# Optimization experiments

Measured on AMD Instinct MI355X. Metric: run time of the kernel, lower is better.

Reference implementation:

```python
import jax, jax.numpy as jnp
import numpy as np
from collections import deque

SIGMA_LOW = 0.02  # TreeFilter2D(sigma=0.02); high-level trees use sigma=1 (low_tree=False)


def bilinear_resize(x, oh, ow):
    # torch F.interpolate(mode='bilinear', align_corners=False)
    B, C, H, W = x.shape
    sy, sx = H / oh, W / ow
    ys = jnp.maximum((jnp.arange(oh, dtype=jnp.float32) + 0.5) * sy - 0.5, 0.0)
    xs = jnp.maximum((jnp.arange(ow, dtype=jnp.float32) + 0.5) * sx - 0.5, 0.0)
    y0 = jnp.clip(jnp.floor(ys).astype(jnp.int32), 0, H - 1)
    x0 = jnp.clip(jnp.floor(xs).astype(jnp.int32), 0, W - 1)
    y1 = jnp.minimum(y0 + 1, H - 1)
    x1 = jnp.minimum(x0 + 1, W - 1)
    wy = (ys - y0).reshape(oh, 1)
    wx = (xs - x0).reshape(1, ow)
    top, bot = x[:, :, y0, :], x[:, :, y1, :]
    v00, v01 = top[:, :, :, x0], top[:, :, :, x1]
    v10, v11 = bot[:, :, :, x0], bot[:, :, :, x1]
    return ((1 - wy) * (1 - wx)) * v00 + ((1 - wy) * wx) * v01 + (wy * (1 - wx)) * v10 + (wy * wx) * v11


def nearest_resize(x, oh, ow):
    B, C, H, W = x.shape
    yi = jnp.minimum((jnp.arange(oh) * (H / oh)).astype(jnp.int32), H - 1)
    xi = jnp.minimum((jnp.arange(ow) * (W / ow)).astype(jnp.int32), W - 1)
    return x[:, :, yi, :][:, :, :, xi]


def _mst_adj(feat, h, w):
    # Kruskal MST on 4-connected grid; edge weight = norm2_distance of features.
    n = h * w
    idx = np.arange(n).reshape(h, w)
    eu = np.concatenate([idx[:, :-1].ravel(), idx[:-1, :].ravel()])
    ev = np.concatenate([idx[:, 1:].ravel(), idx[1:, :].ravel()])
    f = feat.reshape(feat.shape[0], -1).astype(np.float64)
    d = ((f[:, eu] - f[:, ev]) ** 2).sum(axis=0)
    order = np.argsort(d, kind='stable')
    pa = np.arange(n)

    def find(a):
        r = a
        while pa[r] != r:
            r = pa[r]
        while pa[a] != r:
            pa[a], a = r, pa[a]
        return r

    adj = [[] for _ in range(n)]
    cnt = 0
    for e in order:
        u, v = int(eu[e]), int(ev[e])
        ru, rv = find(u), find(v)
        if ru != rv:
            pa[ru] = rv
            adj[u].append(v)
            adj[v].append(u)
            cnt += 1
            if cnt == n - 1:
                break
    return adj


def build_forest(embed):
    # embed: np [B,C,h,w] -> global parent array (ids b*n+i) + per-BFS-level node lists
    B, C, h, w = embed.shape
    n = h * w
    parent = np.arange(B * n)
    level = np.zeros(B * n, dtype=np.int64)
    for b in range(B):
        adj = _mst_adj(embed[b], h, w)
        lv = np.full(n, -1, dtype=np.int64)
        lv[0] = 0
        q = deque([0])
        while q:
            u = q.popleft()
            for v in adj[u]:
                if lv[v] < 0:
                    lv[v] = lv[u] + 1
                    parent[b * n + v] = b * n + u
                    q.append(v)
        level[b * n:(b + 1) * n] = lv
    d = int(level.max())
    levels = [np.nonzero(level == l)[0] for l in range(1, d + 1)]
    return jnp.asarray(parent), levels


def tree_filter(feature, embed, parent, levels, sigma):
    # feature [B,C,n], embed [B,Ce,n]; normalized tree filtering:
    # y_i = sum_j prod(path-edge-weights) x_j / sum_j prod(path-edge-weights)
    B, C, n = feature.shape
    ones = jnp.ones((B, 1, n), feature.dtype)
    xg = jnp.moveaxis(jnp.concatenate([feature, ones], axis=1), 0, 1).reshape(C + 1, B * n)
    eg = jnp.moveaxis(embed, 0, 1).reshape(embed.shape[1], B * n)
    wgt = jnp.exp(-((eg - eg[:, parent]) ** 2).sum(axis=0) / sigma)  # [B*n]; root entries unused
    # upward (leaf->root) subtree aggregation
    A = xg
    for idx in reversed(levels):
        A = A.at[:, parent[idx]].add(wgt[idx] * A[:, idx])
    # downward (root->leaf) completion
    F = A
    for idx in levels:
        F = F.at[:, idx].set(A[:, idx] + wgt[idx] * (F[:, parent[idx]] - wgt[idx] * A[:, idx]))
    y = F[:C] / F[C]
    return jnp.moveaxis(y.reshape(C, B, n), 0, 1)  # [B,C,n]


def setup_inputs() -> dict:
    key = jax.random.key(0)
    ks = jax.random.split(key, 6)
    B, K, h, w = 8, 4, 48, 48
    C = 512
    preds = jax.random.normal(ks[0], (B, K, h, w), jnp.float32)
    low_feats = jax.random.uniform(ks[1], (B, 3, 192, 192), jnp.float32) * 0.1
    hf1 = jax.random.normal(ks[2], (B, C, 24, 24), jnp.float32) * 0.05
    hf2 = jax.random.normal(ks[3], (B, C, 12, 12), jnp.float32) * 0.05
    hf3 = jax.random.normal(ks[4], (B, C, 6, 6), jnp.float32) * 0.05
    rois = (jax.random.uniform(ks[5], (B, 192, 192)) > 0.5).astype(jnp.float32)
    weight = jnp.asarray(0.4, jnp.float32)
    return {"preds": preds, "low_feats": low_feats, "high_feats_1": hf1,
            "high_feats_2": hf2, "high_feats_3": hf3, "unlabeled_ROIs": rois,
            "weight": weight}


def reference(preds, low_feats, high_feats_1, high_feats_2, high_feats_3, unlabeled_ROIs, weight):
    B, K, h, w = preds.shape
    low = bilinear_resize(low_feats, h, w)                     # no_grad in original
    roi = nearest_resize(unlabeled_ROIs[:, None], h, w)        # [B,1,h,w]
    N = roi.sum()
    prob = jax.nn.softmax(preds, axis=1)
    probf = prob.reshape(B, K, -1)
    roif = roi.reshape(B, 1, -1)

    parent0, lv0 = build_forest(np.asarray(low))
    AS = tree_filter(probf, low.reshape(B, low.shape[1], -1), parent0, lv0, SIGMA_LOW)

    loss = jnp.zeros((), preds.dtype)
    for hf in (high_feats_1, high_feats_2, high_feats_3):
        hfi = bilinear_resize(hf, h, w)
        p, lv = build_forest(np.asarray(hfi))
        AS_k = tree_filter(AS, hfi.reshape(B, hfi.shape[1], -1), p, lv, 1.0)
        loss = loss + (roif * jnp.abs(probf - AS_k)).sum()
    loss = jnp.where(N > 0, loss / N, loss)
    return weight * loss
```

## Files before the change

### kernel.cpp

```cpp
#include <hip/hip_runtime.h>
#include <math.h>


#define HH 48
#define WW 48
#define NN (HH*WW)
#define EHH (HH*(WW-1))
#define EEE (2*EHH)
#define BB 8
#define KK 4
#define TPB 256
#define TPE 512
#define TPW 1024
#define TPR 1024
#define TPF 512
#define NPL 5
#define NHE ((EHH+TPE-1)/TPE)
#define ESLOT (4*NN)
#define LVE (2*(NN-1))
#define RIPT ((LVE+TPR-1)/TPR)
#define SENTN 0xFFFFu
#define MAXT 12

#define SSTRIDE_W (4*NN+8)
#define PK_OFF 0
#define D_OFF (4*NN)

__device__ __forceinline__ void edge_uv(int e,int& u,int& v){
  if(e<EHH){ int r=e/(WW-1); int c=e-r*(WW-1); u=r*WW+c; v=u+1; }
  else     { int t=e-EHH; u=t; v=t+WW; }
}

__device__ __forceinline__ void pick_src(int f, const float* lowf, const float* hf1,
                                         const float* hf2, const float* hf3,
                                         const float*& src, int& sh, int& C){
  if(f==0){src=lowf; sh=192; C=3;}
  else if(f==1){src=hf1; sh=24; C=512;}
  else if(f==2){src=hf2; sh=12; C=512;}
  else        {src=hf3; sh=6;  C=512;}
}

__global__ __launch_bounds__(TPB) void k_prob(const float* __restrict__ preds,
                                              float* __restrict__ probf){
  int t=blockIdx.x*TPB+threadIdx.x;
  if(t>=BB*NN) return;
  int b=t/NN, i=t-b*NN;
  const float* p=preds+(size_t)b*KK*NN+i;
  float x0=p[0],x1=p[NN],x2=p[2*NN],x3=p[3*NN];
  float mx=fmaxf(fmaxf(x0,x1),fmaxf(x2,x3));
  float e0=expf(x0-mx),e1=expf(x1-mx),e2=expf(x2-mx),e3=expf(x3-mx);
  float s=((e0+e1)+(e2+e3));
  float* q=probf+(size_t)b*KK*NN+i;
  q[0]=e0/s; q[NN]=e1/s; q[2*NN]=e2/s; q[3*NN]=e3/s;
}

__global__ __launch_bounds__(TPE) void k_edges(
  const float* __restrict__ lowf, const float* __restrict__ hf1,
  const float* __restrict__ hf2, const float* __restrict__ hf3,
  double* __restrict__ pd_low, double* __restrict__ pd_hf, int nchunk)
{
  __shared__ float up[4*NN];
  __shared__ int   y0t[48], y1t[48];
  __shared__ float wyt[48];
  const int tid=threadIdx.x;
  int pidx, chunk, hfidx=0;
  if(blockIdx.x<8){ pidx=blockIdx.x; chunk=0; }
  else { int t=blockIdx.x-8; hfidx=t/nchunk; chunk=t-hfidx*nchunk; pidx=8+hfidx; }
  const int f=pidx>>3, b=pidx&7;
  const float* src; int sh,C;
  pick_src(f,lowf,hf1,hf2,hf3,src,sh,C);
  const int shw=sh*sh;
  const float* srcb=src+(size_t)b*C*shw;
  const int cpc=(f==0)?3:(512/nchunk);
  const int c_begin=chunk*cpc;
  const int c_end=(c_begin+cpc<C)?(c_begin+cpc):C;

  if(tid<48){
    float sy=(float)sh/48.0f;
    float ys=fmaxf(((float)tid+0.5f)*sy-0.5f,0.0f);
    int y0=(int)ys; if(y0>sh-1) y0=sh-1;
    int y1=y0+1; if(y1>sh-1) y1=sh-1;
    y0t[tid]=y0; y1t[tid]=y1; wyt[tid]=ys-(float)y0;
  }

  double accH[NHE], accV[NHE];
  #pragma unroll
  for(int j=0;j<NHE;j++){ accH[j]=0.0; accV[j]=0.0; }

  for(int c0=c_begin;c0<c_end;c0+=4){
    const int nc=(c_end-c0<4)?(c_end-c0):4;
    __syncthreads();
    for(int i=tid;i<NN;i+=TPE){
      int r=i/WW, c=i-r*WW;
      int y0=y0t[r], y1=y1t[r]; float wy=wyt[r];
      int x0=y0t[c], x1=y1t[c]; float wx=wyt[c];
      float w00=(1.0f-wy)*(1.0f-wx), w01=(1.0f-wy)*wx;
      float w10=wy*(1.0f-wx),        w11=wy*wx;
      int o00=y0*sh+x0, o01=y0*sh+x1, o10=y1*sh+x0, o11=y1*sh+x1;
      const float* pl=srcb+(size_t)c0*shw;
      for(int cc=0;cc<nc;cc++){
        const float* p=pl+(size_t)cc*shw;
        up[cc*NN+i]=w00*p[o00]+w01*p[o01]+w10*p[o10]+w11*p[o11];
      }
    }
    __syncthreads();
    for(int j=0;j<NHE;j++){
      int e=tid+j*TPE;
      if(e<EHH){
        int r=e/(WW-1); int u=r*WW+(e-r*(WW-1));
        const float* pu=up+u;
        for(int c=0;c<nc;c++){
          double d=(double)pu[c*NN]-(double)pu[c*NN+1];
          accH[j]=fma(d,d,accH[j]);
        }
      }
    }
    for(int j=0;j<NHE;j++){
      int u=tid+j*TPE;
      if(u<EHH){
        const float* pu=up+u;
        for(int c=0;c<nc;c++){
          double d=(double)pu[c*NN]-(double)pu[c*NN+WW];
          accV[j]=fma(d,d,accV[j]);
        }
      }
    }
  }
  double* outp=(f==0)? pd_low+(size_t)pidx*EEE
                     : pd_hf+((size_t)hfidx*nchunk+chunk)*EEE;
  #pragma unroll
  for(int j=0;j<NHE;j++){
    int e=tid+j*TPE;
    if(e<EHH){ outp[e]=accH[j]; outp[EHH+e]=accV[j]; }
  }
}

__global__ __launch_bounds__(TPB) void k_redux(
  const double* __restrict__ pd_low, const double* __restrict__ pd_hf,
  int nchunk, double* __restrict__ dkeyG)
{
  int t=blockIdx.x*TPB+threadIdx.x;
  if(t>=32*EEE) return;
  int pidx=t/EEE, e=t-pidx*EEE;
  double s;
  if(pidx<8) s=pd_low[(size_t)pidx*EEE+e];
  else {
    const double* p0=pd_hf+((size_t)(pidx-8)*nchunk)*EEE+e;
    s=0.0;
    for(int k=0;k<nchunk;k++) s+=p0[(size_t)k*EEE];
  }
  dkeyG[t]=s;
}

__global__ __launch_bounds__(TPW) void k_boruvka(
  const double* __restrict__ dkeyG,
  float4* __restrict__ adjwG, unsigned char* __restrict__ adjG)
{
  __shared__ double dkey[EEE];
  __shared__ unsigned long long bestd[NN];
  __shared__ int comp[NN];
  __shared__ int lnk[NN];
  __shared__ int beste[NN];
  __shared__ unsigned char mstf[EEE];
  __shared__ int flags[2];

  const int tid=threadIdx.x;
  const int pidx=blockIdx.x;
  const int f=pidx>>3;
  const float sigma=(f==0)?0.02f:1.0f;

  const double* p0=dkeyG+(size_t)pidx*EEE;
  for(int e=tid;e<EEE;e+=TPW) dkey[e]=p0[e];
  for(int i=tid;i<NN;i+=TPW) comp[i]=i;
  for(int e=tid;e<EEE;e+=TPW) mstf[e]=0;
  __syncthreads();

  for(int round=0;round<20;++round){
    for(int i=tid;i<NN;i+=TPW){ bestd[i]=~0ull; beste[i]=0x7fffffff; lnk[i]=i; }
    if(tid==0) flags[1]=0;
    __syncthreads();
    for(int e=tid;e<EEE;e+=TPW){
      int u,v; edge_uv(e,u,v);
      int cu=comp[u], cv=comp[v];
      if(cu!=cv){
        unsigned long long db=(unsigned long long)__double_as_longlong(dkey[e]);
        atomicMin(&bestd[cu],db);
        atomicMin(&bestd[cv],db);
      }
    }
    __syncthreads();
    for(int e=tid;e<EEE;e+=TPW){
      int u,v; edge_uv(e,u,v);
      int cu=comp[u], cv=comp[v];
      if(cu!=cv){
        unsigned long long db=(unsigned long long)__double_as_longlong(dkey[e]);
        if(db==bestd[cu]) atomicMin(&beste[cu],e);
        if(db==bestd[cv]) atomicMin(&beste[cv],e);
      }
    }
    __syncthreads();
    for(int i=tid;i<NN;i+=TPW){
      if(comp[i]==i && beste[i]!=0x7fffffff){
        int e=beste[i]; int u,v; edge_uv(e,u,v);
        int cu=comp[u], cv=comp[v];
        int other=(cu==i)?cv:cu;
        bool mutual=(beste[other]==e);
        if(!mutual || other<i){ lnk[i]=other; mstf[e]=1; flags[1]=1; }
      }
    }
    __syncthreads();
    if(flags[1]==0) break;
    {
      volatile int* vl=lnk;
      for(int i=tid;i<NN;i+=TPW){
        int x=comp[i];
        int p=vl[x];
        int gp=vl[p];
        while(p!=gp){
          vl[x]=gp;
          x=p; p=gp; gp=vl[p];
        }
        comp[i]=p;
      }
    }
    __syncthreads();
  }

  for(int i=tid;i<NN;i+=TPW){
    int r=i/WW, c=i-r*WW;
    int mask=0; float4 w; w.x=0.0f; w.y=0.0f; w.z=0.0f; w.w=0.0f;
    if(c>0    && mstf[r*(WW-1)+c-1]){ mask|=1; w.x=expf(-(float)dkey[r*(WW-1)+c-1]/sigma); }
    if(c<WW-1 && mstf[r*(WW-1)+c])  { mask|=2; w.y=expf(-(float)dkey[r*(WW-1)+c]/sigma); }
    if(r>0    && mstf[EHH+i-WW])    { mask|=4; w.z=expf(-(float)dkey[EHH+i-WW]/sigma); }
    if(r<HH-1 && mstf[EHH+i])       { mask|=8; w.w=expf(-(float)dkey[EHH+i]/sigma); }
    adjwG[(size_t)pidx*NN+i]=w;
    adjG[(size_t)pidx*NN+i]=(unsigned char)mask;
  }
}

__global__ __launch_bounds__(TPR) void k_root(
  const float4* __restrict__ adjwG, const unsigned char* __restrict__ adjG,
  int* __restrict__ sbase)
{
  __shared__ unsigned int eA[ESLOT];
  __shared__ unsigned int eB[ESLOT];
  __shared__ float4 adjwS[NN];
  __shared__ unsigned char adjS[NN];
  __shared__ int chunkS[TPR];
  __shared__ int maxdS;

  const int tid=threadIdx.x;
  const int pidx=blockIdx.x;
  {
    const float4* aw=adjwG+(size_t)pidx*NN;
    for(int t=tid;t<NN;t+=TPR) adjwS[t]=aw[t];
    const int* a4=(const int*)(adjG+(size_t)pidx*NN);
    int* s4=(int*)adjS;
    for(int t=tid;t<NN/4;t+=TPR) s4[t]=a4[t];
  }
  if(tid==0) maxdS=0;
  __syncthreads();

  const int m0=adjS[0];
  const int d0=(m0&1)?0:((m0&2)?1:((m0&4)?2:3));
  const int e0=d0;

  for(int t=tid;t<ESLOT;t+=TPR){
    int u=t>>2, d=t&3;
    unsigned int pk=0;
    if(adjS[u]&(1<<d)){
      int v=(d==0)?u-1:(d==1)?u+1:(d==2)?u-WW:u+WW;
      int rd=d^1;
      int mv=adjS[v];
      int nd=rd;
      #pragma unroll
      for(int k2=4;k2>=1;k2--){ int dd=(rd+k2)&3; if(mv&(1<<dd)) nd=dd; }
      int ne=(v<<2)|nd;
      unsigned int nxt=(ne==e0)?SENTN:(unsigned int)ne;
      pk=(nxt<<16)|1u;
    }
    eA[t]=pk;
  }
  __syncthreads();

  unsigned int* P=eA; unsigned int* Q=eB;
  for(int r2=0;r2<13;r2++){
    for(int t=tid;t<ESLOT;t+=TPR){
      unsigned int pk=P[t];
      unsigned int dist=pk&0xFFFFu, nxt=pk>>16;
      if(dist && nxt!=SENTN){
        unsigned int pk2=P[nxt];
        dist+=pk2&0xFFFFu;
        nxt=pk2>>16;
        pk=(nxt<<16)|dist;
      }
      Q[t]=pk;
    }
    __syncthreads();
    unsigned int* tmp=P; P=Q; Q=tmp;
  }
  for(int t=tid;t<ESLOT;t+=TPR){
    unsigned int dist=P[t]&0xFFFFu;
    Q[t]=dist?(unsigned int)(LVE-(int)dist):0xFFFFFFFFu;
  }
  __syncthreads();

  int* scanA=(int*)P;
  for(int t=tid;t<ESLOT;t+=TPR){
    unsigned int pos=Q[t];
    if(pos!=0xFFFFFFFFu){
      int u=t>>2, d=t&3;
      int v=(d==0)?u-1:(d==1)?u+1:(d==2)?u-WW:u+WW;
      unsigned int rpos=Q[(v<<2)|(d^1)];
      scanA[pos]=(pos<rpos)?1:-1;
    }
  }
  __syncthreads();

  const int base=tid*RIPT;
  int vals[RIPT]; int lsum=0;
  #pragma unroll
  for(int j=0;j<RIPT;j++){
    int p=base+j;
    int v=(p<LVE)?scanA[p]:0;
    lsum+=v; vals[j]=lsum;
  }
  chunkS[tid]=lsum;
  __syncthreads();
  for(int off=1;off<TPR;off<<=1){
    int v=chunkS[tid];
    int vv=(tid>=off)?chunkS[tid-off]:0;
    __syncthreads();
    chunkS[tid]=v+vv;
    __syncthreads();
  }
  const int myoff=(tid>0)?chunkS[tid-1]:0;
  int mymax=0;
  #pragma unroll
  for(int j=0;j<RIPT;j++){
    int p=base+j;
    if(p<LVE){ int s=vals[j]+myoff; scanA[p]=s; if(s>mymax) mymax=s; }
  }
  if(mymax>0) atomicMax(&maxdS,mymax);
  __syncthreads();

  int* sp=sbase+(size_t)pidx*SSTRIDE_W;
  int4* g_pk=(int4*)(sp+PK_OFF);
  if(tid==0){
    g_pk[0]=make_int4(0,__float_as_int(0.0f),0,0);
    sp[D_OFF]=maxdS;
  }
  for(int t=tid;t<ESLOT;t+=TPR){
    unsigned int pos=Q[t];
    if(pos!=0xFFFFFFFFu){
      int u=t>>2, d=t&3;
      int v=(d==0)?u-1:(d==1)?u+1:(d==2)?u-WW:u+WW;
      unsigned int rpos=Q[(v<<2)|(d^1)];
      if(pos<rpos){
        float4 w4=adjwS[u];
        float w=(d==0)?w4.x:(d==1)?w4.y:(d==2)?w4.z:w4.w;
        g_pk[v]=make_int4(u,__float_as_int(w),scanA[pos],0);
      }
    }
  }
}

__global__ __launch_bounds__(TPF) void k_tables(
  const int* __restrict__ sbase, int* __restrict__ ancT,
  float* __restrict__ prodT)
{
  __shared__ int   ancA[NN], ancB[NN];
  __shared__ float prmA[NN], prmB[NN];
  const int tid=threadIdx.x;
  const int pidx=blockIdx.x;
  const int* sp=sbase+(size_t)pidx*SSTRIDE_W;
  const int4* g_pk=(const int4*)(sp+PK_OFF);
  const int maxD=sp[D_OFF];
  int T=1; while((1<<T)<=maxD) T++;
  int* gA=ancT+(size_t)pidx*MAXT*NN;
  float* gP=prodT+(size_t)pidx*MAXT*NN;
  int* aP=ancA; int* aQ=ancB; float* pP=prmA; float* pQ=prmB;
  for(int i=tid;i<NN;i+=TPF){
    int4 rec=g_pk[i];
    aP[i]=rec.x; pP[i]=__int_as_float(rec.y);
    gA[i]=rec.x; gP[i]=pP[i];
  }
  __syncthreads();
  for(int t=1;t<T;t++){
    for(int i=tid;i<NN;i+=TPF){
      int a=aP[i];
      int a2=aP[a]; float pr=pP[i]*pP[a];
      aQ[i]=a2; pQ[i]=pr;
      gA[(size_t)t*NN+i]=a2; gP[(size_t)t*NN+i]=pr;
    }
    __syncthreads();
    { int* t1=aP; aP=aQ; aQ=t1; float* t2=pP; pP=pQ; pQ=t2; }
  }
}

__global__ __launch_bounds__(TPF) void k_fchan(
  const float* __restrict__ X, float* __restrict__ Fout,
  const int* __restrict__ sbase, const int* __restrict__ ancT,
  const float* __restrict__ prodT, int pidx0)
{
  __shared__ float S[NN];
  __shared__ float Sb[NN];
  const int tid=threadIdx.x;
  const int pg=blockIdx.x/5, c=blockIdx.x%5;
  const int pidx=pidx0+pg;
  const int xb=pg&7;
  const int* sp=sbase+(size_t)pidx*SSTRIDE_W;
  const int4* g_pk=(const int4*)(sp+PK_OFF);
  const int maxD=sp[D_OFF];
  int T=1; while((1<<T)<=maxD) T++;
  const int* ancP=ancT+(size_t)pidx*MAXT*NN;
  const float* prmP=prodT+(size_t)pidx*MAXT*NN;

  int dep[NPL]; float wv[NPL];
  #pragma unroll
  for(int j=0;j<NPL;j++){
    int i=tid+j*TPF;
    if(i<NN){
      int4 rec=g_pk[i];
      dep[j]=rec.z; wv[j]=__int_as_float(rec.y);
      S[i]=(c<4)? X[((size_t)xb*KK+c)*NN+i] : 1.0f;
    } else { dep[j]=-1; wv[j]=0.0f; }
  }
  __syncthreads();

  for(int t=0;t<T;t++){
    float sn[NPL]; int aj[NPL]; float pj[NPL];
    #pragma unroll
    for(int j=0;j<NPL;j++){
      int i=tid+j*TPF;
      if(i<NN){ sn[j]=S[i]; aj[j]=ancP[(size_t)t*NN+i]; pj[j]=prmP[(size_t)t*NN+i]; }
      else { sn[j]=0.0f; aj[j]=0; pj[j]=0.0f; }
    }
    __syncthreads();
    int bit=1<<t;
    #pragma unroll
    for(int j=0;j<NPL;j++){
      if(dep[j]>=bit) atomicAdd(&S[aj[j]], pj[j]*sn[j]);
    }
    __syncthreads();
  }

  #pragma unroll
  for(int j=0;j<NPL;j++){
    int i=tid+j*TPF;
    if(i<NN){ float fq=1.0f-wv[j]*wv[j]; Sb[i]=fq*S[i]; }
  }
  __syncthreads();

  float* Sp=Sb; float* Sq=S;
  for(int t=0;t<T;t++){
    float bn[NPL];
    #pragma unroll
    for(int j=0;j<NPL;j++){
      int i=tid+j*TPF;
      if(i<NN){
        int a=ancP[(size_t)t*NN+i]; float ai=prmP[(size_t)t*NN+i];
        bn[j]=fmaf(ai,Sp[a],Sp[i]);
      } else bn[j]=0.0f;
    }
    __syncthreads();
    #pragma unroll
    for(int j=0;j<NPL;j++){
      int i=tid+j*TPF;
      if(i<NN) Sq[i]=bn[j];
    }
    __syncthreads();
    { float* tmp=Sp; Sp=Sq; Sq=tmp; }
  }
  float* o=Fout+(size_t)blockIdx.x*NN;
  for(int i=tid;i<NN;i+=TPF) o[i]=Sp[i];
}

__global__ __launch_bounds__(TPB) void k_div0(const float* __restrict__ FA,
                                              float* __restrict__ AS){
  int t=blockIdx.x*TPB+threadIdx.x;
  if(t>=BB*KK*NN) return;
  int b=t/(KK*NN), rem=t-b*(KK*NN), c=rem/NN, i=rem-c*NN;
  float inv=1.0f/FA[((size_t)b*5+4)*NN+i];
  AS[t]=FA[((size_t)b*5+c)*NN+i]*inv;
}

__global__ __launch_bounds__(TPB) void k_loss(
  const float* __restrict__ FB, const float* __restrict__ probf,
  const float* __restrict__ rois, float* __restrict__ partials)
{
  __shared__ float red[TPB];
  const int tid=threadIdx.x;
  const int fb=blockIdx.x;
  const int b=fb&7;
  const float* pb=probf+(size_t)b*KK*NN;
  float part=0.0f;
  for(int i=tid;i<NN;i+=TPB){
    int r=i/WW, c2=i-r*WW;
    float roi=rois[(size_t)b*(192*192)+(4*r)*192+(4*c2)];
    float inv=1.0f/FB[((size_t)fb*5+4)*NN+i];
    float s=fabsf(pb[i]      -FB[((size_t)fb*5+0)*NN+i]*inv)
          + fabsf(pb[NN+i]   -FB[((size_t)fb*5+1)*NN+i]*inv)
          + fabsf(pb[2*NN+i] -FB[((size_t)fb*5+2)*NN+i]*inv)
          + fabsf(pb[3*NN+i] -FB[((size_t)fb*5+3)*NN+i]*inv);
    part+=roi*s;
  }
  red[tid]=part; __syncthreads();
  for(int s2=TPB/2;s2>0;s2>>=1){ if(tid<s2) red[tid]+=red[tid+s2]; __syncthreads(); }
  if(tid==0) partials[fb]=red[0];
}

__global__ __launch_bounds__(TPB) void k_final(const float* __restrict__ rois,
    const float* __restrict__ partials, const float* __restrict__ wt,
    float* __restrict__ out)
{
  __shared__ float red[TPB];
  const int tid=threadIdx.x;
  float n=0.0f;
  for(int t=tid;t<BB*NN;t+=TPB){
    int b=t/NN, i=t-b*NN; int r=i/WW, c=i-r*WW;
    n += rois[(size_t)b*(192*192)+(4*r)*192+(4*c)];
  }
  red[tid]=n; __syncthreads();
  for(int s=TPB/2;s>0;s>>=1){ if(tid<s) red[tid]+=red[tid+s]; __syncthreads(); }
  if(tid==0){
    float loss=0.0f;
    for(int j=0;j<3*BB;j++) loss+=partials[j];
    float N=red[0];
    out[0]=wt[0]*((N>0.0f)?(loss/N):loss);
  }
}

extern "C" void kernel_launch(void* const* d_in, const int* in_sizes, int n_in,
                              void* d_out, int out_size, void* d_ws, size_t ws_size,
                              hipStream_t stream) {
  (void)in_sizes; (void)n_in; (void)out_size;
  const float* preds=(const float*)d_in[0];
  const float* lowf =(const float*)d_in[1];
  const float* hf1  =(const float*)d_in[2];
  const float* hf2  =(const float*)d_in[3];
  const float* hf3  =(const float*)d_in[4];
  const float* rois =(const float*)d_in[5];
  const float* wt   =(const float*)d_in[6];
  float* out=(float*)d_out;

  char* ws=(char*)d_ws;
  float* partials=(float*)ws;
  float* probf=(float*)(ws+256);
  float* AS   =(float*)(ws+256+(size_t)BB*KK*NN*4);
  size_t sb_off=256+(size_t)2*BB*KK*NN*4;
  int*   sbase=(int*)(ws+sb_off);
  size_t aw_off=sb_off+(size_t)32*SSTRIDE_W*4;
  float4* adjwG=(float4*)(ws+aw_off);
  size_t aj_off=aw_off+(size_t)32*NN*16;
  unsigned char* adjG=(unsigned char*)(ws+aj_off);
  size_t dk_off=aj_off+(size_t)32*NN;
  double* dkeyG=(double*)(ws+dk_off);
  size_t pl_off=dk_off+(size_t)32*EEE*8;
  double* pd_low=(double*)(ws+pl_off);
  size_t ph_off=pl_off+(size_t)8*EEE*8;
  double* pd_hf=(double*)(ws+ph_off);

  int*   ancT =(int*)  (ws+ph_off);
  float* prodT=(float*)(ws+ph_off+(size_t)32*MAXT*NN*4);
  float* FA   =(float*)(ws+ph_off+(size_t)2*32*MAXT*NN*4);
  float* FB   =(float*)(ws+ph_off+(size_t)2*32*MAXT*NN*4+(size_t)40*NN*4);

  int nchunk=32;
  if(ph_off+(size_t)24*32*EEE*8>ws_size) nchunk=16;

  k_prob<<<(BB*NN+TPB-1)/TPB,TPB,0,stream>>>(preds,probf);
  k_edges<<<8+24*nchunk,TPE,0,stream>>>(lowf,hf1,hf2,hf3,pd_low,pd_hf,nchunk);
  k_redux<<<(32*EEE+TPB-1)/TPB,TPB,0,stream>>>(pd_low,pd_hf,nchunk,dkeyG);
  k_boruvka<<<32,TPW,0,stream>>>(dkeyG,adjwG,adjG);
  k_root<<<32,TPR,0,stream>>>(adjwG,adjG,sbase);
  k_tables<<<32,TPF,0,stream>>>(sbase,ancT,prodT);
  k_fchan<<<40,TPF,0,stream>>>(probf,FA,sbase,ancT,prodT,0);
  k_div0<<<(BB*KK*NN+TPB-1)/TPB,TPB,0,stream>>>(FA,AS);
  k_fchan<<<120,TPF,0,stream>>>(AS,FB,sbase,ancT,prodT,8);
  k_loss<<<3*BB,TPB,0,stream>>>(FB,probf,rois,partials);
  k_final<<<1,TPB,0,stream>>>(rois,partials,wt,out);
}
```

Before: 232.6 us.

## Fuse MST, Euler-tour rooting and ancestor tables into one kernel

Merges the Boruvka MST, Euler-tour rooting and binary-lifting table kernels into a single per-tree kernel with one aliased shared-memory arena, so the adjacency masks and weights stay in LDS instead of going through global memory. This removes two launches and their global round trips. Separately, the edge-distance kernel now visits each pixel once and accumulates both its horizontal and vertical edge from the same shared loads. The trade-off is a large shared-memory footprint that limits the kernel to one block per CU, and the ancestor-table phase now runs with 1024 threads instead of 512.

```diff
diff --git a/kernel.cpp b/kernel.cpp
--- a/kernel.cpp
+++ b/kernel.cpp
@@ -12,13 +12,12 @@
 #define TPB 256
 #define TPE 512
 #define TPW 1024
-#define TPR 1024
 #define TPF 512
 #define NPL 5
-#define NHE ((EHH+TPE-1)/TPE)
+#define NPN 5
 #define ESLOT (4*NN)
 #define LVE (2*(NN-1))
-#define RIPT ((LVE+TPR-1)/TPR)
+#define RIPT ((LVE+TPW-1)/TPW)
 #define SENTN 0xFFFFu
 #define MAXT 12
 
@@ -59,7 +58,7 @@
   const float* __restrict__ hf2, const float* __restrict__ hf3,
   double* __restrict__ pd_low, double* __restrict__ pd_hf, int nchunk)
 {
-  __shared__ float up[4*NN];
+  __shared__ float up[4*NN+64];
   __shared__ int   y0t[48], y1t[48];
   __shared__ float wyt[48];
   const int tid=threadIdx.x;
@@ -83,9 +82,9 @@
     y0t[tid]=y0; y1t[tid]=y1; wyt[tid]=ys-(float)y0;
   }
 
-  double accH[NHE], accV[NHE];
+  double accH[NPN], accV[NPN];
   #pragma unroll
-  for(int j=0;j<NHE;j++){ accH[j]=0.0; accV[j]=0.0; }
+  for(int j=0;j<NPN;j++){ accH[j]=0.0; accV[j]=0.0; }
 
   for(int c0=c_begin;c0<c_end;c0+=4){
     const int nc=(c_end-c0<4)?(c_end-c0):4;
@@ -104,24 +103,17 @@
       }
     }
     __syncthreads();
-    for(int j=0;j<NHE;j++){
-      int e=tid+j*TPE;
-      if(e<EHH){
-        int r=e/(WW-1); int u=r*WW+(e-r*(WW-1));
-        const float* pu=up+u;
-        for(int c=0;c<nc;c++){
-          double d=(double)pu[c*NN]-(double)pu[c*NN+1];
-          accH[j]=fma(d,d,accH[j]);
-        }
-      }
-    }
-    for(int j=0;j<NHE;j++){
+    #pragma unroll
+    for(int j=0;j<NPN;j++){
       int u=tid+j*TPE;
-      if(u<EHH){
-        const float* pu=up+u;
-        for(int c=0;c<nc;c++){
-          double d=(double)pu[c*NN]-(double)pu[c*NN+WW];
-          accV[j]=fma(d,d,accV[j]);
+      if(u<NN){
+        int r=u/WW, c=u-r*WW;
+        bool hOK=(c<WW-1), vOK=(r<HH-1);
+        for(int cc=0;cc<nc;cc++){
+          const float* pu=up+cc*NN+u;
+          float a=pu[0], b1=pu[1], c1=pu[WW];
+          if(hOK){ double d=(double)a-(double)b1; accH[j]=fma(d,d,accH[j]); }
+          if(vOK){ double d=(double)a-(double)c1; accV[j]=fma(d,d,accV[j]); }
         }
       }
     }
@@ -129,9 +121,13 @@
   double* outp=(f==0)? pd_low+(size_t)pidx*EEE
                      : pd_hf+((size_t)hfidx*nchunk+chunk)*EEE;
   #pragma unroll
-  for(int j=0;j<NHE;j++){
-    int e=tid+j*TPE;
-    if(e<EHH){ outp[e]=accH[j]; outp[EHH+e]=accV[j]; }
+  for(int j=0;j<NPN;j++){
+    int u=tid+j*TPE;
+    if(u<NN){
+      int r=u/WW, c=u-r*WW;
+      if(c<WW-1) outp[r*(WW-1)+c]=accH[j];
+      if(r<HH-1) outp[EHH+u]=accV[j];
+    }
   }
 }
 
@@ -152,249 +148,236 @@
   dkeyG[t]=s;
 }
 
-__global__ __launch_bounds__(TPW) void k_boruvka(
-  const double* __restrict__ dkeyG,
-  float4* __restrict__ adjwG, unsigned char* __restrict__ adjG)
+__global__ __launch_bounds__(TPW) void k_struct(
+  const double* __restrict__ dkeyG, int* __restrict__ sbase,
+  int* __restrict__ ancT, float* __restrict__ prodT)
 {
-  __shared__ double dkey[EEE];
-  __shared__ unsigned long long bestd[NN];
-  __shared__ int comp[NN];
-  __shared__ int lnk[NN];
-  __shared__ int beste[NN];
-  __shared__ unsigned char mstf[EEE];
-  __shared__ int flags[2];
+  __shared__ __align__(16) char smem[123600];
+  double*             dkey =(double*)(smem+0);
+  unsigned char*      mstf =(unsigned char*)(smem+36096);
+  unsigned long long* bestd=(unsigned long long*)(smem+40608);
+  int*                comp =(int*)(smem+59040);
+  int*                beste=(int*)(smem+68256);
+  int*                lnk  =(int*)(smem+77472);
+  float4*             adjw =(float4*)(smem+40608);
+  unsigned char*      adjS =(unsigned char*)(smem+77472);
+  int*                chunkS=(int*)(smem+79776);
+  unsigned int*       eA   =(unsigned int*)(smem+0);
+  unsigned int*       eB   =(unsigned int*)(smem+86688);
+  int*                flags=(int*)(smem+123552);
+  int*                ancA =(int*)(smem+0);
+  float*              prmA =(float*)(smem+9216);
+  int*                ancB =(int*)(smem+18432);
+  float*              prmB =(float*)(smem+27648);
 
   const int tid=threadIdx.x;
   const int pidx=blockIdx.x;
   const int f=pidx>>3;
   const float sigma=(f==0)?0.02f:1.0f;
 
-  const double* p0=dkeyG+(size_t)pidx*EEE;
-  for(int e=tid;e<EEE;e+=TPW) dkey[e]=p0[e];
-  for(int i=tid;i<NN;i+=TPW) comp[i]=i;
-  for(int e=tid;e<EEE;e+=TPW) mstf[e]=0;
-  __syncthreads();
-
-  for(int round=0;round<20;++round){
-    for(int i=tid;i<NN;i+=TPW){ bestd[i]=~0ull; beste[i]=0x7fffffff; lnk[i]=i; }
-    if(tid==0) flags[1]=0;
-    __syncthreads();
-    for(int e=tid;e<EEE;e+=TPW){
-      int u,v; edge_uv(e,u,v);
-      int cu=comp[u], cv=comp[v];
-      if(cu!=cv){
-        unsigned long long db=(unsigned long long)__double_as_longlong(dkey[e]);
-        atomicMin(&bestd[cu],db);
-        atomicMin(&bestd[cv],db);
-      }
-    }
-    __syncthreads();
-    for(int e=tid;e<EEE;e+=TPW){
-      int u,v; edge_uv(e,u,v);
-      int cu=comp[u], cv=comp[v];
-      if(cu!=cv){
-        unsigned long long db=(unsigned long long)__double_as_longlong(dkey[e]);
-        if(db==bestd[cu]) atomicMin(&beste[cu],e);
-        if(db==bestd[cv]) atomicMin(&beste[cv],e);
-      }
-    }
-    __syncthreads();
+  {
+    const double* p0=dkeyG+(size_t)pidx*EEE;
+    for(int e=tid;e<EEE;e+=TPW) dkey[e]=p0[e];
+    for(int i=tid;i<NN;i+=TPW) comp[i]=i;
+    for(int e=tid;e<EEE;e+=TPW) mstf[e]=0;
+    __syncthreads();
+
+    for(int round=0;round<20;++round){
+      for(int i=tid;i<NN;i+=TPW){ bestd[i]=~0ull; beste[i]=0x7fffffff; lnk[i]=i; }
+      if(tid==0) flags[1]=0;
+      __syncthreads();
+      for(int e=tid;e<EEE;e+=TPW){
+        int u,v; edge_uv(e,u,v);
+        int cu=comp[u], cv=comp[v];
+        if(cu!=cv){
+          unsigned long long db=(unsigned long long)__double_as_longlong(dkey[e]);
+          atomicMin(&bestd[cu],db);
+          atomicMin(&bestd[cv],db);
+        }
+      }
+      __syncthreads();
+      for(int e=tid;e<EEE;e+=TPW){
+        int u,v; edge_uv(e,u,v);
+        int cu=comp[u], cv=comp[v];
+        if(cu!=cv){
+          unsigned long long db=(unsigned long long)__double_as_longlong(dkey[e]);
+          if(db==bestd[cu]) atomicMin(&beste[cu],e);
+          if(db==bestd[cv]) atomicMin(&beste[cv],e);
+        }
+      }
+      __syncthreads();
+      for(int i=tid;i<NN;i+=TPW){
+        if(comp[i]==i && beste[i]!=0x7fffffff){
+          int e=beste[i]; int u,v; edge_uv(e,u,v);
+          int cu=comp[u], cv=comp[v];
+          int other=(cu==i)?cv:cu;
+          bool mutual=(beste[other]==e);
+          if(!mutual || other<i){ lnk[i]=other; mstf[e]=1; flags[1]=1; }
+        }
+      }
+      __syncthreads();
+      if(flags[1]==0) break;
+      {
+        volatile int* vl=lnk;
+        for(int i=tid;i<NN;i+=TPW){
+          int x=comp[i];
+          int p=vl[x];
+          int gp=vl[p];
+          while(p!=gp){
+            vl[x]=gp;
+            x=p; p=gp; gp=vl[p];
+          }
+          comp[i]=p;
+        }
+      }
+      __syncthreads();
+    }
+    __syncthreads();
+
     for(int i=tid;i<NN;i+=TPW){
-      if(comp[i]==i && beste[i]!=0x7fffffff){
-        int e=beste[i]; int u,v; edge_uv(e,u,v);
-        int cu=comp[u], cv=comp[v];
-        int other=(cu==i)?cv:cu;
-        bool mutual=(beste[other]==e);
-        if(!mutual || other<i){ lnk[i]=other; mstf[e]=1; flags[1]=1; }
-      }
-    }
-    __syncthreads();
-    if(flags[1]==0) break;
-    {
-      volatile int* vl=lnk;
+      int r=i/WW, c=i-r*WW;
+      int mask=0; float4 w; w.x=0.0f; w.y=0.0f; w.z=0.0f; w.w=0.0f;
+      if(c>0    && mstf[r*(WW-1)+c-1]){ mask|=1; w.x=expf(-(float)dkey[r*(WW-1)+c-1]/sigma); }
+      if(c<WW-1 && mstf[r*(WW-1)+c])  { mask|=2; w.y=expf(-(float)dkey[r*(WW-1)+c]/sigma); }
+      if(r>0    && mstf[EHH+i-WW])    { mask|=4; w.z=expf(-(float)dkey[EHH+i-WW]/sigma); }
+      if(r<HH-1 && mstf[EHH+i])       { mask|=8; w.w=expf(-(float)dkey[EHH+i]/sigma); }
+      adjw[i]=w;
+      adjS[i]=(unsigned char)mask;
+    }
+    if(tid==0) flags[2]=0;
+    __syncthreads();
+  }
+
+  {
+    const int m0=adjS[0];
+    const int d0=(m0&1)?0:((m0&2)?1:((m0&4)?2:3));
+    const int e0=d0;
+
+    for(int t=tid;t<ESLOT;t+=TPW){
+      int u=t>>2, d=t&3;
+      unsigned int pk=0;
+      if(adjS[u]&(1<<d)){
+        int v=(d==0)?u-1:(d==1)?u+1:(d==2)?u-WW:u+WW;
+        int rd=d^1;
+        int mv=adjS[v];
+        int nd=rd;
+        #pragma unroll
+        for(int k2=4;k2>=1;k2--){ int dd=(rd+k2)&3; if(mv&(1<<dd)) nd=dd; }
+        int ne=(v<<2)|nd;
+        unsigned int nxt=(ne==e0)?SENTN:(unsigned int)ne;
+        pk=(nxt<<16)|1u;
+      }
+      eA[t]=pk;
+    }
+    __syncthreads();
+
+    unsigned int* P=eA; unsigned int* Q=eB;
+    for(int r2=0;r2<13;r2++){
+      for(int t=tid;t<ESLOT;t+=TPW){
+        unsigned int pk=P[t];
+        unsigned int dist=pk&0xFFFFu, nxt=pk>>16;
+        if(dist && nxt!=SENTN){
+          unsigned int pk2=P[nxt];
+          dist+=pk2&0xFFFFu;
+          nxt=pk2>>16;
+          pk=(nxt<<16)|dist;
+        }
+        Q[t]=pk;
+      }
+      __syncthreads();
+      unsigned int* tmp=P; P=Q; Q=tmp;
+    }
+    for(int t=tid;t<ESLOT;t+=TPW){
+      unsigned int dist=P[t]&0xFFFFu;
+      Q[t]=dist?(unsigned int)(LVE-(int)dist):0xFFFFFFFFu;
+    }
+    __syncthreads();
+
+    int* scanA=(int*)P;
+    for(int t=tid;t<ESLOT;t+=TPW){
+      unsigned int pos=Q[t];
+      if(pos!=0xFFFFFFFFu){
+        int u=t>>2, d=t&3;
+        int v=(d==0)?u-1:(d==1)?u+1:(d==2)?u-WW:u+WW;
+        unsigned int rpos=Q[(v<<2)|(d^1)];
+        scanA[pos]=(pos<rpos)?1:-1;
+      }
+    }
+    __syncthreads();
+
+    const int base=tid*RIPT;
+    int vals[RIPT]; int lsum=0;
+    #pragma unroll
+    for(int j=0;j<RIPT;j++){
+      int p=base+j;
+      int v=(p<LVE)?scanA[p]:0;
+      lsum+=v; vals[j]=lsum;
+    }
+    chunkS[tid]=lsum;
+    __syncthreads();
+    for(int off=1;off<TPW;off<<=1){
+      int v=chunkS[tid];
+      int vv=(tid>=off)?chunkS[tid-off]:0;
+      __syncthreads();
+      chunkS[tid]=v+vv;
+      __syncthreads();
+    }
+    const int myoff=(tid>0)?chunkS[tid-1]:0;
+    int mymax=0;
+    #pragma unroll
+    for(int j=0;j<RIPT;j++){
+      int p=base+j;
+      if(p<LVE){ int s=vals[j]+myoff; scanA[p]=s; if(s>mymax) mymax=s; }
+    }
+    if(mymax>0) atomicMax(&flags[2],mymax);
+    __syncthreads();
+
+    int* sp=sbase+(size_t)pidx*SSTRIDE_W;
+    int4* g_pk=(int4*)(sp+PK_OFF);
+    if(tid==0){
+      g_pk[0]=make_int4(0,__float_as_int(0.0f),0,0);
+      sp[D_OFF]=flags[2];
+    }
+    for(int t=tid;t<ESLOT;t+=TPW){
+      unsigned int pos=Q[t];
+      if(pos!=0xFFFFFFFFu){
+        int u=t>>2, d=t&3;
+        int v=(d==0)?u-1:(d==1)?u+1:(d==2)?u-WW:u+WW;
+        unsigned int rpos=Q[(v<<2)|(d^1)];
+        if(pos<rpos){
+          float4 w4=adjw[u];
+          float w=(d==0)?w4.x:(d==1)?w4.y:(d==2)?w4.z:w4.w;
+          g_pk[v]=make_int4(u,__float_as_int(w),scanA[pos],0);
+        }
+      }
+    }
+    __syncthreads();
+  }
+
+  {
+    const int* sp=sbase+(size_t)pidx*SSTRIDE_W;
+    const int4* g_pk=(const int4*)(sp+PK_OFF);
+    const int maxD=flags[2];
+    int T=1; while((1<<T)<=maxD) T++;
+    int* gA=ancT+(size_t)pidx*MAXT*NN;
+    float* gP=prodT+(size_t)pidx*MAXT*NN;
+    int* aP=ancA; int* aQ=ancB; float* pP=prmA; float* pQ=prmB;
+    for(int i=tid;i<NN;i+=TPW){
+      int4 rec=g_pk[i];
+      aP[i]=rec.x; pP[i]=__int_as_float(rec.y);
+      gA[i]=rec.x; gP[i]=pP[i];
+    }
+    __syncthreads();
+    for(int t=1;t<T;t++){
       for(int i=tid;i<NN;i+=TPW){
-        int x=comp[i];
-        int p=vl[x];
-        int gp=vl[p];
-        while(p!=gp){
-          vl[x]=gp;
-          x=p; p=gp; gp=vl[p];
-        }
-        comp[i]=p;
-      }
-    }
-    __syncthreads();
-  }
-
-  for(int i=tid;i<NN;i+=TPW){
-    int r=i/WW, c=i-r*WW;
-    int mask=0; float4 w; w.x=0.0f; w.y=0.0f; w.z=0.0f; w.w=0.0f;
-    if(c>0    && mstf[r*(WW-1)+c-1]){ mask|=1; w.x=expf(-(float)dkey[r*(WW-1)+c-1]/sigma); }
-    if(c<WW-1 && mstf[r*(WW-1)+c])  { mask|=2; w.y=expf(-(float)dkey[r*(WW-1)+c]/sigma); }
-    if(r>0    && mstf[EHH+i-WW])    { mask|=4; w.z=expf(-(float)dkey[EHH+i-WW]/sigma); }
-    if(r<HH-1 && mstf[EHH+i])       { mask|=8; w.w=expf(-(float)dkey[EHH+i]/sigma); }
-    adjwG[(size_t)pidx*NN+i]=w;
-    adjG[(size_t)pidx*NN+i]=(unsigned char)mask;
-  }
-}
-
-__global__ __launch_bounds__(TPR) void k_root(
-  const float4* __restrict__ adjwG, const unsigned char* __restrict__ adjG,
-  int* __restrict__ sbase)
-{
-  __shared__ unsigned int eA[ESLOT];
-  __shared__ unsigned int eB[ESLOT];
-  __shared__ float4 adjwS[NN];
-  __shared__ unsigned char adjS[NN];
-  __shared__ int chunkS[TPR];
-  __shared__ int maxdS;
-
-  const int tid=threadIdx.x;
-  const int pidx=blockIdx.x;
-  {
-    const float4* aw=adjwG+(size_t)pidx*NN;
-    for(int t=tid;t<NN;t+=TPR) adjwS[t]=aw[t];
-    const int* a4=(const int*)(adjG+(size_t)pidx*NN);
-    int* s4=(int*)adjS;
-    for(int t=tid;t<NN/4;t+=TPR) s4[t]=a4[t];
-  }
-  if(tid==0) maxdS=0;
-  __syncthreads();
-
-  const int m0=adjS[0];
-  const int d0=(m0&1)?0:((m0&2)?1:((m0&4)?2:3));
-  const int e0=d0;
-
-  for(int t=tid;t<ESLOT;t+=TPR){
-    int u=t>>2, d=t&3;
-    unsigned int pk=0;
-    if(adjS[u]&(1<<d)){
-      int v=(d==0)?u-1:(d==1)?u+1:(d==2)?u-WW:u+WW;
-      int rd=d^1;
-      int mv=adjS[v];
-      int nd=rd;
-      #pragma unroll
-      for(int k2=4;k2>=1;k2--){ int dd=(rd+k2)&3; if(mv&(1<<dd)) nd=dd; }
-      int ne=(v<<2)|nd;
-      unsigned int nxt=(ne==e0)?SENTN:(unsigned int)ne;
-      pk=(nxt<<16)|1u;
-    }
-    eA[t]=pk;
-  }
-  __syncthreads();
-
-  unsigned int* P=eA; unsigned int* Q=eB;
-  for(int r2=0;r2<13;r2++){
-    for(int t=tid;t<ESLOT;t+=TPR){
-      unsigned int pk=P[t];
-      unsigned int dist=pk&0xFFFFu, nxt=pk>>16;
-      if(dist && nxt!=SENTN){
-        unsigned int pk2=P[nxt];
-        dist+=pk2&0xFFFFu;
-        nxt=pk2>>16;
-        pk=(nxt<<16)|dist;
-      }
-      Q[t]=pk;
-    }
-    __syncthreads();
-    unsigned int* tmp=P; P=Q; Q=tmp;
-  }
-  for(int t=tid;t<ESLOT;t+=TPR){
-    unsigned int dist=P[t]&0xFFFFu;
-    Q[t]=dist?(unsigned int)(LVE-(int)dist):0xFFFFFFFFu;
-  }
-  __syncthreads();
-
-  int* scanA=(int*)P;
-  for(int t=tid;t<ESLOT;t+=TPR){
-    unsigned int pos=Q[t];
-    if(pos!=0xFFFFFFFFu){
-      int u=t>>2, d=t&3;
-      int v=(d==0)?u-1:(d==1)?u+1:(d==2)?u-WW:u+WW;
-      unsigned int rpos=Q[(v<<2)|(d^1)];
-      scanA[pos]=(pos<rpos)?1:-1;
-    }
-  }
-  __syncthreads();
-
-  const int base=tid*RIPT;
-  int vals[RIPT]; int lsum=0;
-  #pragma unroll
-  for(int j=0;j<RIPT;j++){
-    int p=base+j;
-    int v=(p<LVE)?scanA[p]:0;
-    lsum+=v; vals[j]=lsum;
-  }
-  chunkS[tid]=lsum;
-  __syncthreads();
-  for(int off=1;off<TPR;off<<=1){
-    int v=chunkS[tid];
-    int vv=(tid>=off)?chunkS[tid-off]:0;
-    __syncthreads();
-    chunkS[tid]=v+vv;
-    __syncthreads();
-  }
-  const int myoff=(tid>0)?chunkS[tid-1]:0;
-  int mymax=0;
-  #pragma unroll
-  for(int j=0;j<RIPT;j++){
-    int p=base+j;
-    if(p<LVE){ int s=vals[j]+myoff; scanA[p]=s; if(s>mymax) mymax=s; }
-  }
-  if(mymax>0) atomicMax(&maxdS,mymax);
-  __syncthreads();
-
-  int* sp=sbase+(size_t)pidx*SSTRIDE_W;
-  int4* g_pk=(int4*)(sp+PK_OFF);
-  if(tid==0){
-    g_pk[0]=make_int4(0,__float_as_int(0.0f),0,0);
-    sp[D_OFF]=maxdS;
-  }
-  for(int t=tid;t<ESLOT;t+=TPR){
-    unsigned int pos=Q[t];
-    if(pos!=0xFFFFFFFFu){
-      int u=t>>2, d=t&3;
-      int v=(d==0)?u-1:(d==1)?u+1:(d==2)?u-WW:u+WW;
-      unsigned int rpos=Q[(v<<2)|(d^1)];
-      if(pos<rpos){
-        float4 w4=adjwS[u];
-        float w=(d==0)?w4.x:(d==1)?w4.y:(d==2)?w4.z:w4.w;
-        g_pk[v]=make_int4(u,__float_as_int(w),scanA[pos],0);
-      }
-    }
-  }
-}
-
-__global__ __launch_bounds__(TPF) void k_tables(
-  const int* __restrict__ sbase, int* __restrict__ ancT,
-  float* __restrict__ prodT)
-{
-  __shared__ int   ancA[NN], ancB[NN];
-  __shared__ float prmA[NN], prmB[NN];
-  const int tid=threadIdx.x;
-  const int pidx=blockIdx.x;
-  const int* sp=sbase+(size_t)pidx*SSTRIDE_W;
-  const int4* g_pk=(const int4*)(sp+PK_OFF);
-  const int maxD=sp[D_OFF];
-  int T=1; while((1<<T)<=maxD) T++;
-  int* gA=ancT+(size_t)pidx*MAXT*NN;
-  float* gP=prodT+(size_t)pidx*MAXT*NN;
-  int* aP=ancA; int* aQ=ancB; float* pP=prmA; float* pQ=prmB;
-  for(int i=tid;i<NN;i+=TPF){
-    int4 rec=g_pk[i];
-    aP[i]=rec.x; pP[i]=__int_as_float(rec.y);
-    gA[i]=rec.x; gP[i]=pP[i];
-  }
-  __syncthreads();
-  for(int t=1;t<T;t++){
-    for(int i=tid;i<NN;i+=TPF){
-      int a=aP[i];
-      int a2=aP[a]; float pr=pP[i]*pP[a];
-      aQ[i]=a2; pQ[i]=pr;
-      gA[(size_t)t*NN+i]=a2; gP[(size_t)t*NN+i]=pr;
-    }
-    __syncthreads();
-    { int* t1=aP; aP=aQ; aQ=t1; float* t2=pP; pP=pQ; pQ=t2; }
+        int a=aP[i];
+        int a2=aP[a]; float pr=pP[i]*pP[a];
+        aQ[i]=a2; pQ[i]=pr;
+        gA[(size_t)t*NN+i]=a2; gP[(size_t)t*NN+i]=pr;
+      }
+      __syncthreads();
+      { int* t1=aP; aP=aQ; aQ=t1; float* t2=pP; pP=pQ; pQ=t2; }
+    }
   }
 }
 
@@ -550,11 +533,7 @@
   float* AS   =(float*)(ws+256+(size_t)BB*KK*NN*4);
   size_t sb_off=256+(size_t)2*BB*KK*NN*4;
   int*   sbase=(int*)(ws+sb_off);
-  size_t aw_off=sb_off+(size_t)32*SSTRIDE_W*4;
-  float4* adjwG=(float4*)(ws+aw_off);
-  size_t aj_off=aw_off+(size_t)32*NN*16;
-  unsigned char* adjG=(unsigned char*)(ws+aj_off);
-  size_t dk_off=aj_off+(size_t)32*NN;
+  size_t dk_off=sb_off+(size_t)32*SSTRIDE_W*4;
   double* dkeyG=(double*)(ws+dk_off);
   size_t pl_off=dk_off+(size_t)32*EEE*8;
   double* pd_low=(double*)(ws+pl_off);
@@ -572,9 +551,7 @@
   k_prob<<<(BB*NN+TPB-1)/TPB,TPB,0,stream>>>(preds,probf);
   k_edges<<<8+24*nchunk,TPE,0,stream>>>(lowf,hf1,hf2,hf3,pd_low,pd_hf,nchunk);
   k_redux<<<(32*EEE+TPB-1)/TPB,TPB,0,stream>>>(pd_low,pd_hf,nchunk,dkeyG);
-  k_boruvka<<<32,TPW,0,stream>>>(dkeyG,adjwG,adjG);
-  k_root<<<32,TPR,0,stream>>>(adjwG,adjG,sbase);
-  k_tables<<<32,TPF,0,stream>>>(sbase,ancT,prodT);
+  k_struct<<<32,TPW,0,stream>>>(dkeyG,sbase,ancT,prodT);
   k_fchan<<<40,TPF,0,stream>>>(probf,FA,sbase,ancT,prodT,0);
   k_div0<<<(BB*KK*NN+TPB-1)/TPB,TPB,0,stream>>>(FA,AS);
   k_fchan<<<120,TPF,0,stream>>>(AS,FB,sbase,ancT,prodT,8);
```

Measured after the change: 227.0 us. 1.02x faster.
